# Optimization experiments

Measured on AMD Instinct MI355X. Metric: run time of the kernel, lower is better.

## Reference

```python
import jax, jax.numpy as jnp
import numpy as np

B, S, E = 2, 2048, 2048
H, W = 16, 256  # num_heads, window_size
D = E // H      # head_dim = 128


def setup_inputs() -> dict:
    key = jax.random.key(0)
    ks = jax.random.split(key, 9)
    s = 1.0 / np.sqrt(E)
    return {
        "x": jax.random.normal(ks[0], (B, S, E), dtype=jnp.float32),
        "Wq": jax.random.normal(ks[1], (E, E), dtype=jnp.float32) * s,
        "bq": jax.random.normal(ks[2], (E,), dtype=jnp.float32) * 0.01,
        "Wk": jax.random.normal(ks[3], (E, E), dtype=jnp.float32) * s,
        "bk": jax.random.normal(ks[4], (E,), dtype=jnp.float32) * 0.01,
        "Wv": jax.random.normal(ks[5], (E, E), dtype=jnp.float32) * s,
        "bv": jax.random.normal(ks[6], (E,), dtype=jnp.float32) * 0.01,
        "Wo": jax.random.normal(ks[7], (E, E), dtype=jnp.float32) * s,
        "bo": jax.random.normal(ks[8], (E,), dtype=jnp.float32) * 0.01,
    }


def reference(x, Wq, bq, Wk, bk, Wv, bv, Wo, bo):
    Bsz, Sl, _ = x.shape
    # projections -> [B, H, S, D]
    def proj(Wt, bt):
        return (x @ Wt + bt).reshape(Bsz, Sl, H, D).transpose(0, 2, 1, 3)
    q = proj(Wq, bq)
    k = proj(Wk, bk)
    v = proj(Wv, bv)
    # scores [B, H, S, S]
    scores = jnp.einsum("bhqd,bhkd->bhqk", q, k) / jnp.sqrt(jnp.float32(D))
    # causal sliding-window mask: q_pos - W < k_pos <= q_pos
    q_pos = jnp.arange(Sl)[:, None]
    k_pos = jnp.arange(Sl)[None, :]
    valid = (k_pos <= q_pos) & (k_pos > q_pos - W)
    scores = jnp.where(valid, scores, jnp.float32(-jnp.inf))
    attn = jax.nn.softmax(scores, axis=-1)
    ctx = jnp.einsum("bhqk,bhkd->bhqd", attn, v)
    ctx = ctx.transpose(0, 2, 1, 3).reshape(Bsz, Sl, E)
    out = ctx @ Wo + bo
    return out, k, v
```

## Files before the change

kernel.cpp:

```cpp
#include <hip/hip_runtime.h>
#include <hip/hip_bf16.h>

#define SEQ 2048
#define EMB 2048
#define NH 16
#define WIN 256
#define HD 128
#define KDIM 2048
#define NDIM 2048

typedef __bf16 bf16x8 __attribute__((ext_vector_type(8)));
typedef float f32x4 __attribute__((ext_vector_type(4)));

#define MFMA __builtin_amdgcn_mfma_f32_16x16x32_bf16
#define BAR __builtin_amdgcn_s_barrier

__device__ __forceinline__ ushort f2bf(float f) {
  unsigned int x = __float_as_uint(f);
  unsigned int r = (x + 0x7fffu + ((x >> 16) & 1u)) >> 16;
  return (ushort)r;
}

__device__ __forceinline__ void gl16(const ushort* g, ushort* l) {
  __builtin_amdgcn_global_load_lds(
      (const __attribute__((address_space(1))) ushort*)g,
      (__attribute__((address_space(3))) ushort*)l, 16, 0, 0);
}

__global__ __launch_bounds__(256) void xconv_kernel(
    const float* __restrict__ x, ushort* __restrict__ xb) {
  size_t i = ((size_t)blockIdx.x * 256 + threadIdx.x) * 8;
  float4 f0 = *(const float4*)&x[i];
  float4 f1 = *(const float4*)&x[i + 4];
  union { ushort u[8]; uint4 v; } pk;
  pk.u[0] = f2bf(f0.x); pk.u[1] = f2bf(f0.y);
  pk.u[2] = f2bf(f0.z); pk.u[3] = f2bf(f0.w);
  pk.u[4] = f2bf(f1.x); pk.u[5] = f2bf(f1.y);
  pk.u[6] = f2bf(f1.z); pk.u[7] = f2bf(f1.w);
  *(uint4*)&xb[i] = pk.v;
}

__global__ __launch_bounds__(256) void wtrans_kernel(
    const float* __restrict__ w0, const float* __restrict__ w1,
    const float* __restrict__ w2, const float* __restrict__ w3,
    ushort* __restrict__ wt) {
  __shared__ __align__(16) float tf[32 * 132];
  const int t = threadIdx.x;
  const int nblk = blockIdx.x, kblk = blockIdx.y, mat = blockIdx.z;
  const float* Wp = mat == 0 ? w0 : mat == 1 ? w1 : mat == 2 ? w2 : w3;
  const int n0 = nblk * 128, k0 = kblk * 32;
#pragma unroll
  for (int p = 0; p < 4; ++p) {
    int kk = (t >> 5) + 8 * p;
    int nn = (t & 31) * 4;
    float4 v = *(const float4*)&Wp[(size_t)(k0 + kk) * NDIM + n0 + nn];
    *(float4*)&tf[kk * 132 + nn] = v;
  }
  __syncthreads();
  ushort* dst = wt + (size_t)mat * ((size_t)NDIM * KDIM) +
                (size_t)(nblk * 64 + kblk) * 4096;
#pragma unroll
  for (int p = 0; p < 2; ++p) {
    int idx = p * 256 + t;
    int r = idx >> 2, cs = idx & 3;
    int c = cs ^ ((r >> 1) & 3);
    union { ushort u[8]; uint4 v; } pk;
#pragma unroll
    for (int j = 0; j < 8; ++j) pk.u[j] = f2bf(tf[(c * 8 + j) * 132 + r]);
    *(uint4*)&dst[idx * 8] = pk.v;
  }
}

template <int MODE>
__global__ __launch_bounds__(256) void gemm_kernel(
    const ushort* __restrict__ Ab, const ushort* __restrict__ Wt,
    const float* __restrict__ b0, const float* __restrict__ b1,
    const float* __restrict__ b2, float* __restrict__ outF,
    ushort* __restrict__ outQ, ushort* __restrict__ Kbf,
    ushort* __restrict__ vTb) {
  __shared__ __align__(16) ushort As[128 * 32];
  __shared__ __align__(16) ushort Bs[128 * 32];
  const int t = threadIdx.x;
  const int mblk = blockIdx.x, nblk = blockIdx.y, z = blockIdx.z;
  const int m0 = mblk * 128, n0 = nblk * 128;
  const ushort* wtile = Wt + (size_t)z * ((size_t)NDIM * KDIM) +
                        (size_t)(nblk * 64) * 4096;
  const int lane = t & 63, wid = t >> 6;
  const int l15 = lane & 15, lg = lane >> 4;
  const int wm = wid >> 1, wn = wid & 1;
  f32x4 acc[4][4] = {};

  const int slot0 = wid * 128 + lane;
  const int slot1 = slot0 + 64;
  const int r0 = slot0 >> 2, c0 = (slot0 & 3) ^ ((r0 >> 1) & 3);
  const int r1 = slot1 >> 2, c1 = (slot1 & 3) ^ ((r1 >> 1) & 3);
  const ushort* aS0 = Ab + (size_t)(m0 + r0) * KDIM + c0 * 8;
  const ushort* aS1 = Ab + (size_t)(m0 + r1) * KDIM + c1 * 8;
  const ushort* bS0 = wtile + slot0 * 8;
  const ushort* bS1 = wtile + slot1 * 8;
  ushort* aD0 = &As[(wid * 128) * 8];
  ushort* aD1 = &As[(wid * 128 + 64) * 8];
  ushort* bD0 = &Bs[(wid * 128) * 8];
  ushort* bD1 = &Bs[(wid * 128 + 64) * 8];

  for (int kt = 0; kt < KDIM / 32; ++kt) {
    __syncthreads();
    gl16(aS0, aD0); gl16(aS1, aD1);
    gl16(bS0, bD0); gl16(bS1, bD1);
    aS0 += 32; aS1 += 32; bS0 += 4096; bS1 += 4096;
    __syncthreads();
    bf16x8 af[4], bfr[4];
#pragma unroll
    for (int mf = 0; mf < 4; ++mf) {
      int r = wm * 64 + mf * 16 + l15;
      af[mf] = *(const bf16x8*)&As[r * 32 + ((lg ^ ((r >> 1) & 3)) * 8)];
    }
#pragma unroll
    for (int nf = 0; nf < 4; ++nf) {
      int r = wn * 64 + nf * 16 + l15;
      bfr[nf] = *(const bf16x8*)&Bs[r * 32 + ((lg ^ ((r >> 1) & 3)) * 8)];
    }
#pragma unroll
    for (int mf = 0; mf < 4; ++mf)
#pragma unroll
      for (int nf = 0; nf < 4; ++nf)
        acc[mf][nf] = MFMA(af[mf], bfr[nf], acc[mf][nf], 0, 0, 0);
  }

  const float* bias = (MODE == 0) ? b0 : (z == 0 ? b0 : z == 1 ? b1 : b2);
#pragma unroll
  for (int nf = 0; nf < 4; ++nf) {
    int nl = wn * 64 + nf * 16 + l15;
    int n = n0 + nl;
    float bv = bias[n];
#pragma unroll
    for (int mf = 0; mf < 4; ++mf) {
      if (MODE == 0) {
#pragma unroll
        for (int r = 0; r < 4; ++r) {
          int m = m0 + wm * 64 + mf * 16 + lg * 4 + r;
          outF[(size_t)m * NDIM + n] = acc[mf][nf][r] + bv;
        }
      } else {
        int mbase = m0 + wm * 64 + mf * 16 + lg * 4;
        int b = mbase >> 11, sbase = mbase & 2047;
        size_t idx0 = (((size_t)b * NH + nblk) * SEQ + sbase) * HD + nl;
        if (z == 0) {
#pragma unroll
          for (int r = 0; r < 4; ++r)
            outQ[idx0 + (size_t)r * HD] = f2bf(acc[mf][nf][r] + bv);
        } else if (z == 1) {
#pragma unroll
          for (int r = 0; r < 4; ++r) {
            float val = acc[mf][nf][r] + bv;
            outF[(size_t)8388608u + idx0 + (size_t)r * HD] = val;
            Kbf[idx0 + (size_t)r * HD] = f2bf(val);
          }
        } else {
          union { ushort u[4]; uint2 v; } p4;
#pragma unroll
          for (int r = 0; r < 4; ++r) {
            float val = acc[mf][nf][r] + bv;
            outF[(size_t)16777216u + idx0 + (size_t)r * HD] = val;
            p4.u[r] = f2bf(val);
          }
          *(uint2*)&vTb[(((size_t)b * NH + nblk) * HD + nl) * SEQ + sbase] = p4.v;
        }
      }
    }
  }
}

__global__ __launch_bounds__(256) void attn_kernel(
    const ushort* __restrict__ Qb, const ushort* __restrict__ Kb,
    const ushort* __restrict__ vT, ushort* __restrict__ ctx) {
  __shared__ __align__(16) ushort Kl[2][8192];
  __shared__ __align__(16) ushort Vt[2][8192];
  __shared__ __align__(16) ushort Pl[4608];
  const int t = threadIdx.x;
  const int bh = blockIdx.x;
  const int q0 = blockIdx.y * 64;
  const int lane = t & 63, w = t >> 6;
  const int l15 = lane & 15, lg = lane >> 4;
  const int b = bh >> 4, h = bh & 15;
  const ushort* Qbase = Qb + (size_t)bh * SEQ * HD;
  const ushort* Kbase = Kb + (size_t)bh * SEQ * HD;
  const ushort* Vbase = vT + (size_t)bh * HD * SEQ;

  const ushort* kS[4];
  const ushort* vS[4];
#pragma unroll
  for (int p = 0; p < 4; ++p) {
    int s = p * 256 + t;
    int kr = s >> 4, kc = (s & 15) ^ (kr & 7);
    kS[p] = Kbase + kr * HD + kc * 8;
    int vr = s >> 3, vc = (s & 7) ^ (vr & 7);
    vS[p] = Vbase + vr * SEQ + vc * 8;
  }

#define ASTAGE(kt, buf)                                                  \
  {                                                                      \
    size_t ko = (size_t)(kt) * 8192, vo = (size_t)(kt) * 64;             \
    gl16(kS[0] + ko, &Kl[buf][(w * 64) * 8]);                            \
    gl16(kS[1] + ko, &Kl[buf][(256 + w * 64) * 8]);                      \
    gl16(kS[2] + ko, &Kl[buf][(512 + w * 64) * 8]);                      \
    gl16(kS[3] + ko, &Kl[buf][(768 + w * 64) * 8]);                      \
    gl16(vS[0] + vo, &Vt[buf][(w * 64) * 8]);                            \
    gl16(vS[1] + vo, &Vt[buf][(256 + w * 64) * 8]);                      \
    gl16(vS[2] + vo, &Vt[buf][(512 + w * 64) * 8]);                      \
    gl16(vS[3] + vo, &Vt[buf][(768 + w * 64) * 8]);                      \
  }

  bf16x8 aq[4];
#pragma unroll
  for (int ds = 0; ds < 4; ++ds)
    aq[ds] = *(const bf16x8*)&Qbase[(size_t)(q0 + w * 16 + l15) * HD + ds * 32 + lg * 8];

  f32x4 accc[8] = {};
  float mrow[4], lrow[4];
#pragma unroll
  for (int r = 0; r < 4; ++r) { mrow[r] = -1e30f; lrow[r] = 0.f; }

  int ktlo = (q0 - WIN + 1) >> 6;
  if (ktlo < 0) ktlo = 0;
  const int kthi = q0 >> 6;

  ASTAGE(ktlo, 0)
  {
    int t1 = (ktlo + 1 <= kthi) ? ktlo + 1 : kthi;
    ASTAGE(t1, 1)
  }

  for (int kt = ktlo; kt <= kthi; ++kt) {
    const int buf = (kt - ktlo) & 1;
    asm volatile("s_waitcnt vmcnt(8)" ::: "memory");
    BAR();

    f32x4 sacc[4] = {};
#pragma unroll
    for (int ds = 0; ds < 4; ++ds) {
#pragma unroll
      for (int kf = 0; kf < 4; ++kf) {
        int key = kf * 16 + l15;
        bf16x8 kb = *(const bf16x8*)&Kl[buf][key * 128 + (((ds * 4 + lg) ^ (key & 7)) * 8)];
        sacc[kf] = MFMA(aq[ds], kb, sacc[kf], 0, 0, 0);
      }
    }

    const float scale = 0.08838834764831845f;
    const float L2E = 1.4426950408889634f;
#pragma unroll
    for (int r = 0; r < 4; ++r) {
      int q = q0 + w * 16 + lg * 4 + r;
      float sv[4];
      float mx = -1e30f;
#pragma unroll
      for (int kf = 0; kf < 4; ++kf) {
        int key = kt * 64 + kf * 16 + l15;
        float s = sacc[kf][r] * scale;
        bool valid = (key <= q) && (key + WIN > q);
        s = valid ? s : -1e30f;
        sv[kf] = s;
        mx = fmaxf(mx, s);
      }
      mx = fmaxf(mx, __shfl_xor(mx, 1));
      mx = fmaxf(mx, __shfl_xor(mx, 2));
      mx = fmaxf(mx, __shfl_xor(mx, 4));
      mx = fmaxf(mx, __shfl_xor(mx, 8));
      float mnew = fmaxf(mrow[r], mx);
      float sf = exp2f((mrow[r] - mnew) * L2E);
      float ps = 0.f;
#pragma unroll
      for (int kf = 0; kf < 4; ++kf) {
        float p = (sv[kf] > -1e29f) ? exp2f((sv[kf] - mnew) * L2E) : 0.f;
        ps += p;
        Pl[w * 1152 + (lg * 4 + r) * 72 + kf * 16 + l15] = f2bf(p);
      }
      ps += __shfl_xor(ps, 1);
      ps += __shfl_xor(ps, 2);
      ps += __shfl_xor(ps, 4);
      ps += __shfl_xor(ps, 8);
      lrow[r] = lrow[r] * sf + ps;
      mrow[r] = mnew;
#pragma unroll
      for (int nf = 0; nf < 8; ++nf) accc[nf][r] *= sf;
    }

#pragma unroll
    for (int ks = 0; ks < 2; ++ks) {
      bf16x8 pa = *(const bf16x8*)&Pl[w * 1152 + l15 * 72 + ks * 32 + lg * 8];
#pragma unroll
      for (int nf = 0; nf < 8; ++nf) {
        int vr = nf * 16 + l15;
        bf16x8 vb = *(const bf16x8*)&Vt[buf][vr * 64 + (((ks * 4 + lg) ^ (vr & 7)) * 8)];
        accc[nf] = MFMA(pa, vb, accc[nf], 0, 0, 0);
      }
    }

    BAR();
    {
      int ts = (kt + 2 <= kthi) ? kt + 2 : kthi;
      ASTAGE(ts, buf)
    }
  }
#undef ASTAGE

#pragma unroll
  for (int r = 0; r < 4; ++r) {
    int q = q0 + w * 16 + lg * 4 + r;
    float inv = 1.0f / lrow[r];
    size_t rowoff = ((size_t)b * SEQ + q) * EMB + (size_t)h * HD;
#pragma unroll
    for (int nf = 0; nf < 8; ++nf)
      ctx[rowoff + nf * 16 + l15] = f2bf(accc[nf][r] * inv);
  }
}

extern "C" void kernel_launch(void* const* d_in, const int* in_sizes, int n_in,
                              void* d_out, int out_size, void* d_ws, size_t ws_size,
                              hipStream_t stream) {
  const float* x  = (const float*)d_in[0];
  const float* Wq = (const float*)d_in[1];
  const float* bq = (const float*)d_in[2];
  const float* Wk = (const float*)d_in[3];
  const float* bk = (const float*)d_in[4];
  const float* Wv = (const float*)d_in[5];
  const float* bv = (const float*)d_in[6];
  const float* Wo = (const float*)d_in[7];
  const float* bo = (const float*)d_in[8];
  float* out = (float*)d_out;
  ushort* ws = (ushort*)d_ws;
  ushort* Wt   = ws;
  ushort* Qb   = ws + 16777216;
  ushort* Kbf  = ws + 25165824;
  ushort* vTb  = ws + 33554432;
  ushort* xb   = ws + 41943040;
  ushort* ctxb = xb;

  xconv_kernel<<<4096, 256, 0, stream>>>(x, xb);
  wtrans_kernel<<<dim3(16, 64, 4), 256, 0, stream>>>(Wq, Wk, Wv, Wo, Wt);
  gemm_kernel<1><<<dim3(32, 16, 3), 256, 0, stream>>>(xb, Wt, bq, bk, bv, out,
                                                      Qb, Kbf, vTb);
  attn_kernel<<<dim3(32, 32), 256, 0, stream>>>(Qb, Kbf, vTb, ctxb);
  gemm_kernel<0><<<dim3(32, 16, 1), 256, 0, stream>>>(
      ctxb, Wt + (size_t)3 * 4194304, bo, nullptr, nullptr, out, nullptr,
      nullptr, nullptr);
}
```

Measured before the change: 248.3 us.

## Move V transpose into separate kernel and remap attention blocks for XCD locality

Removes the strided transposed bf16 V store from the QKV GEMM epilogue and adds a dedicated kernel that transposes the fp32 V output through shared memory with coalesced writes. The attention grid becomes 1D with a remapping so blocks of the same batch-head land on the same XCD, aiming to improve L2 reuse of K/V. This costs an extra launch and an extra read of the fp32 V tensor.

```diff
diff --git a/kernel.cpp b/kernel.cpp
--- a/kernel.cpp
+++ b/kernel.cpp
@@ -71,13 +71,39 @@
   }
 }
 
+__global__ __launch_bounds__(256) void vtrans_kernel(
+    const float* __restrict__ Vf, ushort* __restrict__ vT) {
+  __shared__ float tf[64 * 129];
+  const int t = threadIdx.x;
+  const int s0 = blockIdx.x * 64, bh = blockIdx.y;
+  const float* src = Vf + ((size_t)bh * SEQ + s0) * HD;
+#pragma unroll
+  for (int p = 0; p < 8; ++p) {
+    int idx = p * 256 + t;
+    int s = idx >> 5, c4 = (idx & 31) * 4;
+    float4 v = *(const float4*)&src[(size_t)s * HD + c4];
+    float* d = &tf[s * 129 + c4];
+    d[0] = v.x; d[1] = v.y; d[2] = v.z; d[3] = v.w;
+  }
+  __syncthreads();
+  ushort* dst = vT + (size_t)bh * HD * SEQ + s0;
+#pragma unroll
+  for (int p = 0; p < 4; ++p) {
+    int slot = p * 256 + t;
+    int d = slot >> 3, c = slot & 7;
+    union { ushort u[8]; uint4 v; } pk;
+#pragma unroll
+    for (int j = 0; j < 8; ++j) pk.u[j] = f2bf(tf[(c * 8 + j) * 129 + d]);
+    *(uint4*)&dst[(size_t)d * SEQ + c * 8] = pk.v;
+  }
+}
+
 template <int MODE>
 __global__ __launch_bounds__(256) void gemm_kernel(
     const ushort* __restrict__ Ab, const ushort* __restrict__ Wt,
     const float* __restrict__ b0, const float* __restrict__ b1,
     const float* __restrict__ b2, float* __restrict__ outF,
-    ushort* __restrict__ outQ, ushort* __restrict__ Kbf,
-    ushort* __restrict__ vTb) {
+    ushort* __restrict__ outQ, ushort* __restrict__ Kbf) {
   __shared__ __align__(16) ushort As[128 * 32];
   __shared__ __align__(16) ushort Bs[128 * 32];
   const int t = threadIdx.x;
@@ -135,36 +161,23 @@
     float bv = bias[n];
 #pragma unroll
     for (int mf = 0; mf < 4; ++mf) {
-      if (MODE == 0) {
-#pragma unroll
-        for (int r = 0; r < 4; ++r) {
-          int m = m0 + wm * 64 + mf * 16 + lg * 4 + r;
-          outF[(size_t)m * NDIM + n] = acc[mf][nf][r] + bv;
-        }
-      } else {
-        int mbase = m0 + wm * 64 + mf * 16 + lg * 4;
-        int b = mbase >> 11, sbase = mbase & 2047;
-        size_t idx0 = (((size_t)b * NH + nblk) * SEQ + sbase) * HD + nl;
-        if (z == 0) {
-#pragma unroll
-          for (int r = 0; r < 4; ++r)
-            outQ[idx0 + (size_t)r * HD] = f2bf(acc[mf][nf][r] + bv);
-        } else if (z == 1) {
-#pragma unroll
-          for (int r = 0; r < 4; ++r) {
-            float val = acc[mf][nf][r] + bv;
-            outF[(size_t)8388608u + idx0 + (size_t)r * HD] = val;
-            Kbf[idx0 + (size_t)r * HD] = f2bf(val);
+#pragma unroll
+      for (int r = 0; r < 4; ++r) {
+        int m = m0 + wm * 64 + mf * 16 + lg * 4 + r;
+        float val = acc[mf][nf][r] + bv;
+        if (MODE == 0) {
+          outF[(size_t)m * NDIM + n] = val;
+        } else {
+          int b = m >> 11, s = m & 2047;
+          size_t idx = (((size_t)b * NH + nblk) * SEQ + s) * HD + nl;
+          if (z == 0) {
+            outQ[idx] = f2bf(val);
+          } else if (z == 1) {
+            outF[(size_t)8388608u + idx] = val;
+            Kbf[idx] = f2bf(val);
+          } else {
+            outF[(size_t)16777216u + idx] = val;
           }
-        } else {
-          union { ushort u[4]; uint2 v; } p4;
-#pragma unroll
-          for (int r = 0; r < 4; ++r) {
-            float val = acc[mf][nf][r] + bv;
-            outF[(size_t)16777216u + idx0 + (size_t)r * HD] = val;
-            p4.u[r] = f2bf(val);
-          }
-          *(uint2*)&vTb[(((size_t)b * NH + nblk) * HD + nl) * SEQ + sbase] = p4.v;
         }
       }
     }
@@ -178,8 +191,9 @@
   __shared__ __align__(16) ushort Vt[2][8192];
   __shared__ __align__(16) ushort Pl[4608];
   const int t = threadIdx.x;
-  const int bh = blockIdx.x;
-  const int q0 = blockIdx.y * 64;
+  const int bid = blockIdx.x;
+  const int bh = (bid & 7) * 4 + (bid >> 8);
+  const int q0 = ((bid >> 3) & 31) * 64;
   const int lane = t & 63, w = t >> 6;
   const int l15 = lane & 15, lg = lane >> 4;
   const int b = bh >> 4, h = bh & 15;
@@ -340,9 +354,10 @@
   xconv_kernel<<<4096, 256, 0, stream>>>(x, xb);
   wtrans_kernel<<<dim3(16, 64, 4), 256, 0, stream>>>(Wq, Wk, Wv, Wo, Wt);
   gemm_kernel<1><<<dim3(32, 16, 3), 256, 0, stream>>>(xb, Wt, bq, bk, bv, out,
-                                                      Qb, Kbf, vTb);
-  attn_kernel<<<dim3(32, 32), 256, 0, stream>>>(Qb, Kbf, vTb, ctxb);
+                                                      Qb, Kbf);
+  vtrans_kernel<<<dim3(32, 32), 256, 0, stream>>>(out + 16777216, vTb);
+  attn_kernel<<<1024, 256, 0, stream>>>(Qb, Kbf, vTb, ctxb);
   gemm_kernel<0><<<dim3(32, 16, 1), 256, 0, stream>>>(
       ctxb, Wt + (size_t)3 * 4194304, bo, nullptr, nullptr, out, nullptr,
-      nullptr, nullptr);
-}
+      nullptr);
+}
```

After: 256.2 us. 1.03x slower.
